# Kernel optimization log

Measured on AMD Instinct MI355X. Metric: run time of the kernel, lower is better.

## Reference

```python
import jax, jax.numpy as jnp
from jax import lax
import numpy as np

BLOCK = 128  # chunk size for the chunked linear-attention recurrence


def setup_inputs() -> dict:
    key = jax.random.key(0)
    kq, kk, kv, ks = jax.random.split(key, 4)
    B, H, N, D = 2, 16, 4096, 128
    q = jax.random.normal(kq, (B, H, N, D), dtype=jnp.float32)
    k = jax.random.normal(kk, (B, H, N, D), dtype=jnp.float32)
    v = jax.random.normal(kv, (B, H, N, D), dtype=jnp.float32)
    s = jax.random.uniform(ks, (H, 1, 1), dtype=jnp.float32)  # positive decay slopes per head
    return {"q": q, "k": k, "v": v, "s": s}


def reference(q, k, v, s):
    # Lightning attention: o_t = q_t @ (sum_{i<=t} exp(-s*(t-i)) k_i v_i^T)
    # computed in chunks of BLOCK with a carried D x D state per (batch, head).
    B, H, N, D = q.shape
    nb = N // BLOCK
    sl = s.reshape(H, 1, 1)                                   # (H,1,1)
    idx = jnp.arange(BLOCK, dtype=q.dtype)
    diff = idx[:, None] - idx[None, :]                        # t - i
    intra_decay = jnp.where(diff >= 0, jnp.exp(-sl * diff), 0.0)   # (H,BLOCK,BLOCK)
    q_decay = jnp.exp(-sl * idx[:, None])                     # (H,BLOCK,1): lambda^tau
    k_decay = jnp.exp(-sl * (BLOCK - idx[:, None]))           # (H,BLOCK,1): lambda^(BLOCK-tau)
    block_decay = jnp.exp(-s.reshape(1, H, 1, 1) * BLOCK)     # (1,H,1,1): lambda^BLOCK

    # (nb, B, H, BLOCK, D) so lax.scan iterates over chunks
    qb = q.reshape(B, H, nb, BLOCK, D).transpose(2, 0, 1, 3, 4)
    kb = k.reshape(B, H, nb, BLOCK, D).transpose(2, 0, 1, 3, 4)
    vb = v.reshape(B, H, nb, BLOCK, D).transpose(2, 0, 1, 3, 4)

    def step(S, blk):
        qi, ki, vi = blk                                      # each (B,H,BLOCK,D)
        scores = jnp.einsum('bhtd,bhsd->bhts', qi, ki) * intra_decay
        o_intra = jnp.einsum('bhts,bhsd->bhtd', scores, vi)
        o_inter = jnp.einsum('bhtd,bhde->bhte', qi * q_decay, S)
        S_new = block_decay * S + jnp.einsum('bhsd,bhse->bhde', ki * k_decay, vi)
        return S_new, o_intra + o_inter

    S0 = jnp.zeros((B, H, D, D), dtype=q.dtype)
    _, ob = lax.scan(step, S0, (qb, kb, vb))                  # (nb,B,H,BLOCK,D)
    return ob.transpose(1, 2, 0, 3, 4).reshape(B, H, N, D)
```

## Files before the change

### kernel.cpp

```cpp
#include <hip/hip_runtime.h>
#include <hip/hip_bf16.h>


#define LDB   136
#define NB    32
#define HH    16
#define NSEQ  4096

typedef float  f32x4  __attribute__((ext_vector_type(4)));
typedef __bf16 bf16x8 __attribute__((ext_vector_type(8)));
typedef unsigned short u16x8 __attribute__((ext_vector_type(8)));
typedef unsigned short u16x4 __attribute__((ext_vector_type(4)));

__device__ __forceinline__ unsigned short f2bf(float f) {
  unsigned int u = __float_as_uint(f);
  unsigned int r = (u + 0x7fffu + ((u >> 16) & 1u)) >> 16;
  return (unsigned short)r;
}
__device__ __forceinline__ float bf2f(unsigned short h) {
  return __uint_as_float(((unsigned int)h) << 16);
}
__device__ __forceinline__ bf16x8 cvt8(float4 a, float4 b) {
  bf16x8 r;
  r[0] = (__bf16)a.x; r[1] = (__bf16)a.y; r[2] = (__bf16)a.z; r[3] = (__bf16)a.w;
  r[4] = (__bf16)b.x; r[5] = (__bf16)b.y; r[6] = (__bf16)b.z; r[7] = (__bf16)b.w;
  return r;
}

__device__ __forceinline__ void stage_transpose512(const float* __restrict__ src,
                                                   unsigned short* dst, int tid) {
#pragma unroll
  for (int i = 0; i < 8; ++i) {
    int idx = i * 512 + tid;
    int d   = idx & 127;
    int tq  = idx >> 7;
    u16x4 w;
#pragma unroll
    for (int j = 0; j < 4; ++j)
      w[j] = f2bf(src[(tq * 4 + j) * 128 + d]);
    *reinterpret_cast<u16x4*>(dst + d * LDB + tq * 4) = w;
  }
}

__device__ __forceinline__ void stage_transpose_scaled512(const float* __restrict__ src,
                                                          unsigned short* dst, int tid,
                                                          float sl) {
#pragma unroll
  for (int i = 0; i < 8; ++i) {
    int idx = i * 512 + tid;
    int d   = idx & 127;
    int tq  = idx >> 7;
    u16x4 w;
#pragma unroll
    for (int j = 0; j < 4; ++j) {
      int tau = tq * 4 + j;
      float kd = __expf(-sl * (float)(128 - tau));
      w[j] = f2bf(src[tau * 128 + d] * kd);
    }
    *reinterpret_cast<u16x4*>(dst + d * LDB + tq * 4) = w;
  }
}

template <int M>
__device__ __forceinline__ void mmT(const unsigned short* A, const unsigned short* BT,
                                    int lane, int wr, int wc, f32x4 acc[M][4]) {
  const int lr = lane & 15;
  const int lg = lane >> 4;
#pragma unroll
  for (int kk = 0; kk < 4; ++kk) {
    const int kb = kk * 32 + lg * 8;
    bf16x8 af[M], bf_[4];
#pragma unroll
    for (int m = 0; m < M; ++m) {
      u16x8 raw = *reinterpret_cast<const u16x8*>(A + (wr + m * 16 + lr) * LDB + kb);
      af[m] = __builtin_bit_cast(bf16x8, raw);
    }
#pragma unroll
    for (int n = 0; n < 4; ++n) {
      u16x8 raw = *reinterpret_cast<const u16x8*>(BT + (wc + n * 16 + lr) * LDB + kb);
      bf_[n] = __builtin_bit_cast(bf16x8, raw);
    }
#pragma unroll
    for (int m = 0; m < M; ++m)
#pragma unroll
      for (int n = 0; n < 4; ++n)
        acc[m][n] = __builtin_amdgcn_mfma_f32_16x16x32_bf16(af[m], bf_[n], acc[m][n], 0, 0, 0);
  }
}

__global__ __launch_bounds__(512, 4) void la_kv(const float* __restrict__ k,
                                                const float* __restrict__ v,
                                                const float* __restrict__ s,
                                                unsigned short* __restrict__ ws) {
  __shared__ __align__(16) unsigned short kTs[128 * LDB];
  __shared__ __align__(16) unsigned short vT[128 * LDB];
  const int tid = threadIdx.x;
  const int bid = blockIdx.x;
  const int c   = bid & (NB - 1);
  const int bh  = bid >> 5;
  const float sl = s[bh & (HH - 1)];
  const size_t base = ((size_t)bh * NSEQ + (size_t)c * 128) * 128;

  stage_transpose_scaled512(k + base, kTs, tid, sl);
  stage_transpose512(v + base, vT, tid);
  __syncthreads();

  const int wid = tid >> 6, lane = tid & 63;
  const int wr = (wid >> 1) * 32, wc = (wid & 1) * 64;
  const int lr = lane & 15, lg = lane >> 4;

  f32x4 acc[2][4];
#pragma unroll
  for (int m = 0; m < 2; ++m)
#pragma unroll
    for (int n = 0; n < 4; ++n)
      acc[m][n] = (f32x4)0.f;

  mmT<2>(vT, kTs, lane, wr, wc, acc);

  unsigned short* dst = ws + ((size_t)bh * NB + c) * 16384;
#pragma unroll
  for (int m = 0; m < 2; ++m)
#pragma unroll
    for (int n = 0; n < 4; ++n)
#pragma unroll
      for (int r = 0; r < 4; ++r)
        dst[(wr + m * 16 + lg * 4 + r) * 128 + (wc + n * 16 + lr)] = f2bf(acc[m][n][r]);
}

__global__ __launch_bounds__(256) void la_scan(const float* __restrict__ s,
                                               unsigned short* __restrict__ ws) {
  const int t   = blockIdx.x * 256 + threadIdx.x;
  const int bh  = t >> 12;
  const int de4 = (t & 4095) * 4;
  const float bd = __expf(-s[bh & (HH - 1)] * 128.f);
  unsigned short* p = ws + (size_t)bh * NB * 16384 + de4;
  float st[4] = {0.f, 0.f, 0.f, 0.f};
#pragma unroll
  for (int c = 0; c < NB; ++c) {
    u16x4 w = *reinterpret_cast<u16x4*>(p + c * 16384);
    u16x4 o;
#pragma unroll
    for (int j = 0; j < 4; ++j) {
      float tmp = bf2f(w[j]);
      o[j] = f2bf(st[j]);
      st[j] = st[j] * bd + tmp;
    }
    *reinterpret_cast<u16x4*>(p + c * 16384) = o;
  }
}

__global__ __launch_bounds__(512, 4) void la_out(const float* __restrict__ q,
                                                 const float* __restrict__ k,
                                                 const float* __restrict__ v,
                                                 const float* __restrict__ s,
                                                 const unsigned short* __restrict__ ws,
                                                 float* __restrict__ out) {
  __shared__ __align__(16) unsigned short Pb[128 * LDB];
  __shared__ __align__(16) unsigned short vT[128 * LDB];
  const int tid = threadIdx.x;
  const int bid = blockIdx.x;
  const int c   = bid & (NB - 1);
  const int bh  = bid >> 5;
  const float sl = s[bh & (HH - 1)];
  const size_t base = ((size_t)bh * NSEQ + (size_t)c * 128) * 128;

  stage_transpose512(v + base, vT, tid);

  const int wid = tid >> 6, lane = tid & 63;
  const int wr = (wid >> 1) * 32, wc = (wid & 1) * 64;
  const int lr = lane & 15, lg = lane >> 4;

  f32x4 accS[2][4];
#pragma unroll
  for (int m = 0; m < 2; ++m)
#pragma unroll
    for (int n = 0; n < 4; ++n)
      accS[m][n] = (f32x4)0.f;

  bf16x8 qf[4][2];
#pragma unroll
  for (int kk = 0; kk < 4; ++kk) {
    const int kb = kk * 32 + lg * 8;
#pragma unroll
    for (int m = 0; m < 2; ++m) {
      const float* p = q + base + (size_t)(wr + m * 16 + lr) * 128 + kb;
      qf[kk][m] = cvt8(*reinterpret_cast<const float4*>(p),
                       *reinterpret_cast<const float4*>(p + 4));
    }
    bf16x8 kf[4];
#pragma unroll
    for (int n = 0; n < 4; ++n) {
      const float* p = k + base + (size_t)(wc + n * 16 + lr) * 128 + kb;
      kf[n] = cvt8(*reinterpret_cast<const float4*>(p),
                   *reinterpret_cast<const float4*>(p + 4));
    }
#pragma unroll
    for (int m = 0; m < 2; ++m)
#pragma unroll
      for (int n = 0; n < 4; ++n)
        accS[m][n] = __builtin_amdgcn_mfma_f32_16x16x32_bf16(qf[kk][m], kf[n], accS[m][n], 0, 0, 0);
  }

#pragma unroll
  for (int m = 0; m < 2; ++m)
#pragma unroll
    for (int n = 0; n < 4; ++n)
#pragma unroll
      for (int r = 0; r < 4; ++r) {
        int t  = wr + m * 16 + lg * 4 + r;
        int sc = wc + n * 16 + lr;
        float pv = (t >= sc) ? accS[m][n][r] * __expf(-sl * (float)(t - sc)) : 0.f;
        Pb[t * LDB + sc] = f2bf(pv);
      }

  const unsigned short* Sp = ws + ((size_t)bh * NB + c) * 16384;
  f32x4 acc2[2][4];
#pragma unroll
  for (int m = 0; m < 2; ++m)
#pragma unroll
    for (int n = 0; n < 4; ++n)
      acc2[m][n] = (f32x4)0.f;

#pragma unroll
  for (int kk = 0; kk < 4; ++kk) {
    const int kb = kk * 32 + lg * 8;
    bf16x8 sf[4];
#pragma unroll
    for (int n = 0; n < 4; ++n) {
      u16x8 raw = *reinterpret_cast<const u16x8*>(Sp + (size_t)(wc + n * 16 + lr) * 128 + kb);
      sf[n] = __builtin_bit_cast(bf16x8, raw);
    }
#pragma unroll
    for (int m = 0; m < 2; ++m)
#pragma unroll
      for (int n = 0; n < 4; ++n)
        acc2[m][n] = __builtin_amdgcn_mfma_f32_16x16x32_bf16(qf[kk][m], sf[n], acc2[m][n], 0, 0, 0);
  }

#pragma unroll
  for (int m = 0; m < 2; ++m)
#pragma unroll
    for (int r = 0; r < 4; ++r) {
      float qd = __expf(-sl * (float)(wr + m * 16 + lg * 4 + r));
#pragma unroll
      for (int n = 0; n < 4; ++n)
        acc2[m][n][r] *= qd;
    }

  __syncthreads();

  mmT<2>(Pb, vT, lane, wr, wc, acc2);

#pragma unroll
  for (int m = 0; m < 2; ++m)
#pragma unroll
    for (int n = 0; n < 4; ++n)
#pragma unroll
      for (int r = 0; r < 4; ++r)
        out[base + (size_t)(wr + m * 16 + lg * 4 + r) * 128 + (wc + n * 16 + lr)] =
            acc2[m][n][r];
}

extern "C" void kernel_launch(void* const* d_in, const int* in_sizes, int n_in,
                              void* d_out, int out_size, void* d_ws, size_t ws_size,
                              hipStream_t stream) {
  const float* q = (const float*)d_in[0];
  const float* k = (const float*)d_in[1];
  const float* v = (const float*)d_in[2];
  const float* s = (const float*)d_in[3];
  float* out = (float*)d_out;
  unsigned short* ws = (unsigned short*)d_ws;

  la_kv<<<dim3(2 * HH * NB), dim3(512), 0, stream>>>(k, v, s, ws);
  la_scan<<<dim3(2 * HH * 16384 / 4 / 256), dim3(256), 0, stream>>>(s, ws);
  la_out<<<dim3(2 * HH * NB), dim3(512), 0, stream>>>(q, k, v, s, ws, out);
}
```

Baseline: 121.7 us.

## Stash transposed bf16 V in workspace and restructure la_out to 256 threads

```diff
diff --git a/kernel.cpp b/kernel.cpp
--- a/kernel.cpp
+++ b/kernel.cpp
@@ -4,6 +4,7 @@
 
 #define LDB   136
 #define NB    32
+#define NG    16
 #define HH    16
 #define NSEQ  4096
 
@@ -61,37 +62,11 @@
   }
 }
 
-template <int M>
-__device__ __forceinline__ void mmT(const unsigned short* A, const unsigned short* BT,
-                                    int lane, int wr, int wc, f32x4 acc[M][4]) {
-  const int lr = lane & 15;
-  const int lg = lane >> 4;
-#pragma unroll
-  for (int kk = 0; kk < 4; ++kk) {
-    const int kb = kk * 32 + lg * 8;
-    bf16x8 af[M], bf_[4];
-#pragma unroll
-    for (int m = 0; m < M; ++m) {
-      u16x8 raw = *reinterpret_cast<const u16x8*>(A + (wr + m * 16 + lr) * LDB + kb);
-      af[m] = __builtin_bit_cast(bf16x8, raw);
-    }
-#pragma unroll
-    for (int n = 0; n < 4; ++n) {
-      u16x8 raw = *reinterpret_cast<const u16x8*>(BT + (wc + n * 16 + lr) * LDB + kb);
-      bf_[n] = __builtin_bit_cast(bf16x8, raw);
-    }
-#pragma unroll
-    for (int m = 0; m < M; ++m)
-#pragma unroll
-      for (int n = 0; n < 4; ++n)
-        acc[m][n] = __builtin_amdgcn_mfma_f32_16x16x32_bf16(af[m], bf_[n], acc[m][n], 0, 0, 0);
-  }
-}
-
 __global__ __launch_bounds__(512, 4) void la_kv(const float* __restrict__ k,
                                                 const float* __restrict__ v,
                                                 const float* __restrict__ s,
-                                                unsigned short* __restrict__ ws) {
+                                                unsigned short* __restrict__ vtws,
+                                                unsigned short* __restrict__ kvws) {
   __shared__ __align__(16) unsigned short kTs[128 * LDB];
   __shared__ __align__(16) unsigned short vT[128 * LDB];
   const int tid = threadIdx.x;
@@ -116,9 +91,26 @@
     for (int n = 0; n < 4; ++n)
       acc[m][n] = (f32x4)0.f;
 
-  mmT<2>(vT, kTs, lane, wr, wc, acc);
-
-  unsigned short* dst = ws + ((size_t)bh * NB + c) * 16384;
+#pragma unroll
+  for (int kk = 0; kk < 4; ++kk) {
+    const int kb = kk * 32 + lg * 8;
+    bf16x8 af[2], bf_[4];
+#pragma unroll
+    for (int m = 0; m < 2; ++m)
+      af[m] = __builtin_bit_cast(bf16x8,
+          *reinterpret_cast<const u16x8*>(vT + (wr + m * 16 + lr) * LDB + kb));
+#pragma unroll
+    for (int n = 0; n < 4; ++n)
+      bf_[n] = __builtin_bit_cast(bf16x8,
+          *reinterpret_cast<const u16x8*>(kTs + (wc + n * 16 + lr) * LDB + kb));
+#pragma unroll
+    for (int m = 0; m < 2; ++m)
+#pragma unroll
+      for (int n = 0; n < 4; ++n)
+        acc[m][n] = __builtin_amdgcn_mfma_f32_16x16x32_bf16(af[m], bf_[n], acc[m][n], 0, 0, 0);
+  }
+
+  unsigned short* dst = kvws + ((size_t)bh * NB + c) * 16384;
 #pragma unroll
   for (int m = 0; m < 2; ++m)
 #pragma unroll
@@ -126,15 +118,24 @@
 #pragma unroll
       for (int r = 0; r < 4; ++r)
         dst[(wr + m * 16 + lg * 4 + r) * 128 + (wc + n * 16 + lr)] = f2bf(acc[m][n][r]);
+
+  unsigned short* vdst = vtws + ((size_t)bh * NB + c) * 16384;
+#pragma unroll
+  for (int i = 0; i < 4; ++i) {
+    int linear = (i * 512 + tid) * 8;
+    int r = linear >> 7, cc = linear & 127;
+    *reinterpret_cast<u16x8*>(vdst + linear) =
+        *reinterpret_cast<const u16x8*>(vT + r * LDB + cc);
+  }
 }
 
 __global__ __launch_bounds__(256) void la_scan(const float* __restrict__ s,
-                                               unsigned short* __restrict__ ws) {
+                                               unsigned short* __restrict__ kvws) {
   const int t   = blockIdx.x * 256 + threadIdx.x;
   const int bh  = t >> 12;
   const int de4 = (t & 4095) * 4;
   const float bd = __expf(-s[bh & (HH - 1)] * 128.f);
-  unsigned short* p = ws + (size_t)bh * NB * 16384 + de4;
+  unsigned short* p = kvws + (size_t)bh * NB * 16384 + de4;
   float st[4] = {0.f, 0.f, 0.f, 0.f};
 #pragma unroll
   for (int c = 0; c < NB; ++c) {
@@ -150,14 +151,13 @@
   }
 }
 
-__global__ __launch_bounds__(512, 4) void la_out(const float* __restrict__ q,
+__global__ __launch_bounds__(256, 4) void la_out(const float* __restrict__ q,
                                                  const float* __restrict__ k,
-                                                 const float* __restrict__ v,
                                                  const float* __restrict__ s,
-                                                 const unsigned short* __restrict__ ws,
+                                                 const unsigned short* __restrict__ vtws,
+                                                 const unsigned short* __restrict__ kvws,
                                                  float* __restrict__ out) {
   __shared__ __align__(16) unsigned short Pb[128 * LDB];
-  __shared__ __align__(16) unsigned short vT[128 * LDB];
   const int tid = threadIdx.x;
   const int bid = blockIdx.x;
   const int c   = bid & (NB - 1);
@@ -165,17 +165,18 @@
   const float sl = s[bh & (HH - 1)];
   const size_t base = ((size_t)bh * NSEQ + (size_t)c * 128) * 128;
 
-  stage_transpose512(v + base, vT, tid);
-
   const int wid = tid >> 6, lane = tid & 63;
-  const int wr = (wid >> 1) * 32, wc = (wid & 1) * 64;
+  const int wr = wid * 32;
   const int lr = lane & 15, lg = lane >> 4;
 
-  f32x4 accS[2][4];
-#pragma unroll
-  for (int m = 0; m < 2; ++m)
-#pragma unroll
-    for (int n = 0; n < 4; ++n)
+  const unsigned short* vch = vtws + ((size_t)bh * NB + c) * 16384;
+  const unsigned short* Sp  = kvws + ((size_t)bh * NB + c) * 16384;
+
+  f32x4 accS[2][8];
+#pragma unroll
+  for (int m = 0; m < 2; ++m)
+#pragma unroll
+    for (int n = 0; n < 8; ++n)
       accS[m][n] = (f32x4)0.f;
 
   bf16x8 qf[4][2];
@@ -188,54 +189,47 @@
       qf[kk][m] = cvt8(*reinterpret_cast<const float4*>(p),
                        *reinterpret_cast<const float4*>(p + 4));
     }
-    bf16x8 kf[4];
-#pragma unroll
-    for (int n = 0; n < 4; ++n) {
-      const float* p = k + base + (size_t)(wc + n * 16 + lr) * 128 + kb;
-      kf[n] = cvt8(*reinterpret_cast<const float4*>(p),
-                   *reinterpret_cast<const float4*>(p + 4));
-    }
-#pragma unroll
-    for (int m = 0; m < 2; ++m)
-#pragma unroll
-      for (int n = 0; n < 4; ++n)
-        accS[m][n] = __builtin_amdgcn_mfma_f32_16x16x32_bf16(qf[kk][m], kf[n], accS[m][n], 0, 0, 0);
-  }
-
-#pragma unroll
-  for (int m = 0; m < 2; ++m)
-#pragma unroll
-    for (int n = 0; n < 4; ++n)
+#pragma unroll
+    for (int n = 0; n < 8; ++n) {
+      const float* p = k + base + (size_t)(n * 16 + lr) * 128 + kb;
+      bf16x8 kf = cvt8(*reinterpret_cast<const float4*>(p),
+                       *reinterpret_cast<const float4*>(p + 4));
+#pragma unroll
+      for (int m = 0; m < 2; ++m)
+        accS[m][n] = __builtin_amdgcn_mfma_f32_16x16x32_bf16(qf[kk][m], kf, accS[m][n], 0, 0, 0);
+    }
+  }
+
+#pragma unroll
+  for (int m = 0; m < 2; ++m)
+#pragma unroll
+    for (int n = 0; n < 8; ++n)
 #pragma unroll
       for (int r = 0; r < 4; ++r) {
         int t  = wr + m * 16 + lg * 4 + r;
-        int sc = wc + n * 16 + lr;
+        int sc = n * 16 + lr;
         float pv = (t >= sc) ? accS[m][n][r] * __expf(-sl * (float)(t - sc)) : 0.f;
         Pb[t * LDB + sc] = f2bf(pv);
       }
 
-  const unsigned short* Sp = ws + ((size_t)bh * NB + c) * 16384;
-  f32x4 acc2[2][4];
-#pragma unroll
-  for (int m = 0; m < 2; ++m)
-#pragma unroll
-    for (int n = 0; n < 4; ++n)
-      acc2[m][n] = (f32x4)0.f;
-
-#pragma unroll
-  for (int kk = 0; kk < 4; ++kk) {
-    const int kb = kk * 32 + lg * 8;
-    bf16x8 sf[4];
-#pragma unroll
-    for (int n = 0; n < 4; ++n) {
-      u16x8 raw = *reinterpret_cast<const u16x8*>(Sp + (size_t)(wc + n * 16 + lr) * 128 + kb);
-      sf[n] = __builtin_bit_cast(bf16x8, raw);
-    }
-#pragma unroll
-    for (int m = 0; m < 2; ++m)
-#pragma unroll
-      for (int n = 0; n < 4; ++n)
-        acc2[m][n] = __builtin_amdgcn_mfma_f32_16x16x32_bf16(qf[kk][m], sf[n], acc2[m][n], 0, 0, 0);
+  f32x4 oi[2][8];
+#pragma unroll
+  for (int m = 0; m < 2; ++m)
+#pragma unroll
+    for (int n = 0; n < 8; ++n)
+      oi[m][n] = (f32x4)0.f;
+
+#pragma unroll
+  for (int kk = 0; kk < 4; ++kk) {
+    const int kb = kk * 32 + lg * 8;
+#pragma unroll
+    for (int n = 0; n < 8; ++n) {
+      bf16x8 sf = __builtin_bit_cast(bf16x8,
+          *reinterpret_cast<const u16x8*>(Sp + (size_t)(n * 16 + lr) * 128 + kb));
+#pragma unroll
+      for (int m = 0; m < 2; ++m)
+        oi[m][n] = __builtin_amdgcn_mfma_f32_16x16x32_bf16(qf[kk][m], sf, oi[m][n], 0, 0, 0);
+    }
   }
 
 #pragma unroll
@@ -244,22 +238,36 @@
     for (int r = 0; r < 4; ++r) {
       float qd = __expf(-sl * (float)(wr + m * 16 + lg * 4 + r));
 #pragma unroll
-      for (int n = 0; n < 4; ++n)
-        acc2[m][n][r] *= qd;
-    }
-
-  __syncthreads();
-
-  mmT<2>(Pb, vT, lane, wr, wc, acc2);
-
-#pragma unroll
-  for (int m = 0; m < 2; ++m)
-#pragma unroll
-    for (int n = 0; n < 4; ++n)
+      for (int n = 0; n < 8; ++n)
+        oi[m][n][r] *= qd;
+    }
+
+#pragma unroll
+  for (int kk = 0; kk < 4; ++kk) {
+    const int kb = kk * 32 + lg * 8;
+    bf16x8 pa[2];
+#pragma unroll
+    for (int m = 0; m < 2; ++m)
+      pa[m] = __builtin_bit_cast(bf16x8,
+          *reinterpret_cast<const u16x8*>(Pb + (wr + m * 16 + lr) * LDB + kb));
+#pragma unroll
+    for (int n = 0; n < 8; ++n) {
+      bf16x8 vb = __builtin_bit_cast(bf16x8,
+          *reinterpret_cast<const u16x8*>(vch + (size_t)(n * 16 + lr) * 128 + kb));
+#pragma unroll
+      for (int m = 0; m < 2; ++m)
+        oi[m][n] = __builtin_amdgcn_mfma_f32_16x16x32_bf16(pa[m], vb, oi[m][n], 0, 0, 0);
+    }
+  }
+
+#pragma unroll
+  for (int m = 0; m < 2; ++m)
+#pragma unroll
+    for (int n = 0; n < 8; ++n)
 #pragma unroll
       for (int r = 0; r < 4; ++r)
-        out[base + (size_t)(wr + m * 16 + lg * 4 + r) * 128 + (wc + n * 16 + lr)] =
-            acc2[m][n][r];
+        __builtin_nontemporal_store(oi[m][n][r],
+            out + base + (size_t)(wr + m * 16 + lg * 4 + r) * 128 + (n * 16 + lr));
 }
 
 extern "C" void kernel_launch(void* const* d_in, const int* in_sizes, int n_in,
@@ -270,9 +278,10 @@
   const float* v = (const float*)d_in[2];
   const float* s = (const float*)d_in[3];
   float* out = (float*)d_out;
-  unsigned short* ws = (unsigned short*)d_ws;
-
-  la_kv<<<dim3(2 * HH * NB), dim3(512), 0, stream>>>(k, v, s, ws);
-  la_scan<<<dim3(2 * HH * 16384 / 4 / 256), dim3(256), 0, stream>>>(s, ws);
-  la_out<<<dim3(2 * HH * NB), dim3(512), 0, stream>>>(q, k, v, s, ws, out);
-}
+  unsigned short* vtws = (unsigned short*)d_ws;
+  unsigned short* kvws = vtws + (size_t)32 * NB * 16384;
+
+  la_kv<<<dim3(2 * HH * NB), dim3(512), 0, stream>>>(k, v, s, vtws, kvws);
+  la_scan<<<dim3(2 * HH * 16384 / 4 / 256), dim3(256), 0, stream>>>(s, kvws);
+  la_out<<<dim3(2 * HH * NB), dim3(256), 0, stream>>>(q, k, s, vtws, kvws, out);
+}
```

Result: slower. 140.4 us (+15.3%).
